# Optimization experiments

Measured on AMD Instinct MI355X. Metric: run time of the kernel, lower is better.

Reference implementation:

```python
import jax, jax.numpy as jnp
import numpy as np
from jax import lax

D_MODEL = 64
D_STATE = 128
D_INNER = 128  # d_model * expand_factor; must equal D_STATE for the original code to broadcast
BATCH = 4
SEQ = 1024
LN_EPS = 1e-5


def setup_inputs() -> dict:
    key = jax.random.key(0)
    ks = jax.random.split(key, 12)
    s = 0.05
    return {
        "x": jax.random.normal(ks[0], (BATCH, SEQ, D_MODEL), jnp.float32),
        "W_in": jax.random.normal(ks[1], (2 * D_INNER, D_MODEL), jnp.float32) * s,
        "W_delta": jax.random.normal(ks[2], (D_INNER, D_MODEL), jnp.float32) * s,
        "b_delta": jax.random.normal(ks[3], (D_INNER,), jnp.float32) * s,
        "W_B": jax.random.normal(ks[4], (D_STATE, D_MODEL), jnp.float32) * s,
        "b_B": jax.random.normal(ks[5], (D_STATE,), jnp.float32) * s,
        "W_C": jax.random.normal(ks[6], (D_STATE, D_MODEL), jnp.float32) * s,
        "b_C": jax.random.normal(ks[7], (D_STATE,), jnp.float32) * s,
        "A": jax.random.normal(ks[8], (D_INNER, D_STATE), jnp.float32) * 0.01,
        "W_out": jax.random.normal(ks[9], (D_MODEL, D_INNER), jnp.float32) * s,
        "ln_w": jnp.ones((D_MODEL,), jnp.float32),
        "ln_b": jnp.zeros((D_MODEL,), jnp.float32),
    }


def _layer_norm(x, w, b):
    mu = x.mean(-1, keepdims=True)
    var = ((x - mu) ** 2).mean(-1, keepdims=True)
    return (x - mu) * lax.rsqrt(var + LN_EPS) * w + b


def reference(x, W_in, W_delta, b_delta, W_B, b_B, W_C, b_C, A, W_out, ln_w, ln_b):
    # projections
    xp = jnp.einsum('bld,ed->ble', x, W_in)            # (B, L, 2*d_inner)
    x_ssm, gate = xp[..., :D_INNER], xp[..., D_INNER:]
    delta = jax.nn.softplus(jnp.einsum('bld,id->bli', x, W_delta) + b_delta)  # (B, L, d_inner)
    Bm = jnp.einsum('bld,sd->bls', x, W_B) + b_B        # (B, L, d_state)
    Cm = jnp.einsum('bld,sd->bls', x, W_C) + b_C        # (B, L, d_state)

    # A_discrete.mean(dim=1): mean over d_inner of exp(delta * A)
    Abar = jnp.exp(delta[..., :, None] * A).mean(axis=2)  # (B, L, d_state)
    x_pool = x_ssm.mean(axis=-1)                          # (B, L) mean over d_inner
    Bx = Bm * x_pool[..., None]                           # (B, L, d_state)

    def step(h, inp):
        a_t, bx_t, c_t = inp                              # each (B, d_state)
        h = a_t * h + bx_t
        y = (c_t * h).sum(axis=-1)                        # (B,)
        return h, y

    h0 = jnp.zeros((x.shape[0], D_STATE), x.dtype)
    _, ys = lax.scan(step, h0,
                     (jnp.swapaxes(Abar, 0, 1), jnp.swapaxes(Bx, 0, 1), jnp.swapaxes(Cm, 0, 1)))
    y = jnp.swapaxes(ys, 0, 1)[..., None]                 # (B, L, 1) -> broadcast over d_inner

    y = y * jax.nn.silu(gate)                             # (B, L, d_inner)
    out = jnp.einsum('bli,di->bld', y, W_out)             # (B, L, d_model)
    return _layer_norm(out + x, ln_w, ln_b)
```

## Files before the change

### kernel.cpp

```cpp
#include <hip/hip_runtime.h>
#include <math.h>

#define NB   4
#define SL   1024
#define NTOK (NB*SL)
#define DM   64
#define DI   128
#define DSt  128
#define SEGLEN 16
#define NSEG (SL/SEGLEN)

#define OFF_GATE   0
#define OFF_DELTA  (OFF_GATE  + NTOK*DI)
#define OFF_BM     (OFF_DELTA + NTOK*DI)
#define OFF_CM     (OFF_BM    + NTOK*DSt)
#define OFF_XPOOL  (OFF_CM    + NTOK*DSt)
#define OFF_ABAR   (OFF_XPOOL + NTOK)
#define OFF_Y      (OFF_ABAR  + NTOK*DSt)
#define OFF_HEND   (OFF_DELTA)
#define OFF_P      (OFF_DELTA + NB*NSEG*DSt)

#define PROJ_TG   128
#define PROJ_TOK  (NTOK/PROJ_TG)

static __device__ __forceinline__ float wave64_sum(float v) {
#pragma unroll
    for (int m = 32; m >= 1; m >>= 1) v += __shfl_xor(v, m, 64);
    return v;
}

__global__ __launch_bounds__(256) void k_proj(
    const float* __restrict__ x, const float* __restrict__ W_in,
    const float* __restrict__ W_delta, const float* __restrict__ b_delta,
    const float* __restrict__ W_B, const float* __restrict__ b_B,
    const float* __restrict__ W_C, const float* __restrict__ b_C,
    float* __restrict__ ws)
{
    __shared__ float xl[PROJ_TOK*DM];
    const int tid = threadIdx.x;
    const int l   = tid & 63;
    const int w   = tid >> 6;
    const int cat = blockIdx.x >> 7;
    const int tg  = blockIdx.x & (PROJ_TG-1);
    const int tok0 = tg * PROJ_TOK;

    {
        const float4* xg = (const float4*)(x + tok0*DM);
        float4* xl4 = (float4*)xl;
        xl4[tid]       = xg[tid];
        xl4[tid + 256] = xg[tid + 256];
    }
    __syncthreads();

    const float* Wbase; const float* bias; float* dst;
    if      (cat == 0) { Wbase = W_in + DI*DM; bias = nullptr; dst = ws + OFF_GATE;  }
    else if (cat == 1) { Wbase = W_delta;      bias = b_delta; dst = ws + OFF_DELTA; }
    else if (cat == 2) { Wbase = W_B;          bias = b_B;     dst = ws + OFF_BM;    }
    else               { Wbase = W_C;          bias = b_C;     dst = ws + OFF_CM;    }

    float4 w0[16], w1[16];
    {
        const float4* Wr0 = (const float4*)(Wbase + l*DM);
        const float4* Wr1 = (const float4*)(Wbase + (l+64)*DM);
#pragma unroll
        for (int k = 0; k < 16; ++k) { w0[k] = Wr0[k]; w1[k] = Wr1[k]; }
    }
    float bias0 = 0.f, bias1 = 0.f;
    if (bias) { bias0 = bias[l]; bias1 = bias[l+64]; }

#pragma unroll 2
    for (int it = 0; it < PROJ_TOK/4; ++it) {
        const int tl = it*4 + w;
        float a0=0.f,a1=0.f,a2=0.f,a3=0.f, c0=0.f,c1=0.f,c2=0.f,c3=0.f;
#pragma unroll
        for (int k = 0; k < 16; ++k) {
            const float4 xv = *(const float4*)(xl + tl*DM + 4*k);
            a0 = fmaf(w0[k].x, xv.x, a0);
            a1 = fmaf(w0[k].y, xv.y, a1);
            a2 = fmaf(w0[k].z, xv.z, a2);
            a3 = fmaf(w0[k].w, xv.w, a3);
            c0 = fmaf(w1[k].x, xv.x, c0);
            c1 = fmaf(w1[k].y, xv.y, c1);
            c2 = fmaf(w1[k].z, xv.z, c2);
            c3 = fmaf(w1[k].w, xv.w, c3);
        }
        float ra = (a0+a1) + (a2+a3) + bias0;
        float rb = (c0+c1) + (c2+c3) + bias1;
        if (cat == 1) {
            ra = fmaxf(ra, 0.f) + log1pf(__expf(-fabsf(ra)));
            rb = fmaxf(rb, 0.f) + log1pf(__expf(-fabsf(rb)));
        }
        const int tok = tok0 + tl;
        dst[tok*128 + l]      = ra;
        dst[tok*128 + 64 + l] = rb;
    }

    if (cat == 0) {
        float wp = 0.f;
#pragma unroll 8
        for (int i = 0; i < DI; ++i) wp += W_in[i*DM + l];
        wp *= (1.0f/DI);
#pragma unroll
        for (int it = 0; it < PROJ_TOK/4; ++it) {
            const int tl = it*4 + w;
            float v = xl[tl*DM + l] * wp;
            v = wave64_sum(v);
            if (l == 0) ws[OFF_XPOOL + tok0 + tl] = v;
        }
    }
}

__global__ __launch_bounds__(256, 2) void k_abar(const float* __restrict__ A,
                                                 float* __restrict__ ws)
{
    const int tid  = threadIdx.x;
    const int s    = tid & 127;
    const int half = tid >> 7;
    float areg[DI];
#pragma unroll
    for (int i = 0; i < DI; ++i) areg[i] = A[i*DSt + s];

    const float* delta = ws + OFF_DELTA;
    float*       Abar  = ws + OFF_ABAR;
    const int base = blockIdx.x * 8 + half * 4;
#pragma unroll
    for (int p = 0; p < 4; ++p) {
        const int tok = base + p;
        const float* dv = delta + tok*DI;
        float a0 = 0.f, a1 = 0.f, a2 = 0.f, a3 = 0.f;
#pragma unroll
        for (int i4 = 0; i4 < DI/4; ++i4) {
            const float4 d4 = *(const float4*)(dv + 4*i4);
            a0 += __expf(d4.x * areg[4*i4    ]);
            a1 += __expf(d4.y * areg[4*i4 + 1]);
            a2 += __expf(d4.z * areg[4*i4 + 2]);
            a3 += __expf(d4.w * areg[4*i4 + 3]);
        }
        Abar[tok*DSt + s] = ((a0+a1) + (a2+a3)) * (1.0f/DI);
    }
}

__global__ __launch_bounds__(128) void k_scan1(float* __restrict__ ws)
{
    const int s   = threadIdx.x;
    const int b   = blockIdx.x >> 6;
    const int seg = blockIdx.x & 63;
    const float* Abar  = ws + OFF_ABAR;
    const float* Bm    = ws + OFF_BM;
    const float* xpool = ws + OFF_XPOOL;
    float h = 0.f, p = 1.f;
    const int t0 = b*SL + seg*SEGLEN;
#pragma unroll
    for (int t = 0; t < SEGLEN; ++t) {
        const float a  = Abar[(t0 + t)*DSt + s];
        const float bx = Bm[(t0 + t)*DSt + s] * xpool[t0 + t];
        h = fmaf(a, h, bx);
        p *= a;
    }
    ws[OFF_HEND + blockIdx.x*DSt + s] = h;
    ws[OFF_P    + blockIdx.x*DSt + s] = p;
}

__global__ __launch_bounds__(128) void k_scan2(float* __restrict__ ws)
{
    __shared__ float prod[SEGLEN][132];
    const int s   = threadIdx.x;
    const int b   = blockIdx.x >> 6;
    const int seg = blockIdx.x & 63;
    const float* Abar  = ws + OFF_ABAR;
    const float* Bm    = ws + OFF_BM;
    const float* Cm    = ws + OFF_CM;
    const float* xpool = ws + OFF_XPOOL;
    const float* hend  = ws + OFF_HEND;
    const float* P     = ws + OFF_P;

    float h = 0.f;
#pragma unroll 4
    for (int j = 0; j < seg; ++j) {
        const int idx = (b*NSEG + j)*DSt + s;
        h = fmaf(P[idx], h, hend[idx]);
    }
    const int t0 = b*SL + seg*SEGLEN;
#pragma unroll
    for (int t = 0; t < SEGLEN; ++t) {
        const float a  = Abar[(t0 + t)*DSt + s];
        const float bx = Bm[(t0 + t)*DSt + s] * xpool[t0 + t];
        h = fmaf(a, h, bx);
        prod[t][s] = Cm[(t0 + t)*DSt + s] * h;
    }
    __syncthreads();
    const int t = s >> 3, r = s & 7;
    float4 acc4 = {0.f,0.f,0.f,0.f};
#pragma unroll
    for (int k4 = 0; k4 < 4; ++k4) {
        const float4 v = *(const float4*)(&prod[t][r*16 + 4*k4]);
        acc4.x += v.x; acc4.y += v.y; acc4.z += v.z; acc4.w += v.w;
    }
    float acc = (acc4.x + acc4.y) + (acc4.z + acc4.w);
#pragma unroll
    for (int m = 1; m <= 4; m <<= 1) acc += __shfl_xor(acc, m, 64);
    if (r == 0) ws[OFF_Y + b*SL + seg*SEGLEN + t] = acc;
}

__global__ __launch_bounds__(256) void k_out(
    const float* __restrict__ x, const float* __restrict__ W_out,
    const float* __restrict__ ln_w, const float* __restrict__ ln_b,
    const float* __restrict__ ws, float* __restrict__ out)
{
    __shared__ float4 Wl[DM*32];
    __shared__ float vbuf[4][DI];
    const int tid = threadIdx.x;
    const int d   = tid & 63;
    const int wv  = tid >> 6;

    const float4* W4g = (const float4*)W_out;
#pragma unroll
    for (int j = 0; j < 8; ++j) {
        const int f = tid + j*256;
        const int row = f >> 5, c4 = f & 31;
        Wl[row*32 + (c4 ^ (row & 7))] = W4g[f];
    }
    __syncthreads();

    const float* gate = ws + OFF_GATE;
    const float* y    = ws + OFF_Y;
    const float lw = ln_w[d], lb = ln_b[d];

#pragma unroll
    for (int it = 0; it < 4; ++it) {
        const int tok = blockIdx.x*16 + it*4 + wv;
        const float yt = y[tok];
        const float g0 = gate[tok*DI + d];
        const float g1 = gate[tok*DI + 64 + d];
        vbuf[wv][d]      = yt * (g0 / (1.f + __expf(-g0)));
        vbuf[wv][64 + d] = yt * (g1 / (1.f + __expf(-g1)));

        float ac0 = 0.f, ac1 = 0.f, ac2 = 0.f, ac3 = 0.f;
#pragma unroll 8
        for (int q = 0; q < 32; ++q) {
            const float4 w  = Wl[d*32 + (q ^ (d & 7))];
            const float4 vv = *(const float4*)(&vbuf[wv][q*4]);
            ac0 = fmaf(w.x, vv.x, ac0);
            ac1 = fmaf(w.y, vv.y, ac1);
            ac2 = fmaf(w.z, vv.z, ac2);
            ac3 = fmaf(w.w, vv.w, ac3);
        }
        const float z  = (ac0+ac1) + (ac2+ac3) + x[tok*DM + d];
        const float s1 = wave64_sum(z);
        const float s2 = wave64_sum(z*z);
        const float mu  = s1 * (1.f/64.f);
        const float var = s2 * (1.f/64.f) - mu*mu;
        out[tok*DM + d] = (z - mu) * rsqrtf(var + 1e-5f) * lw + lb;
    }
}

extern "C" void kernel_launch(void* const* d_in, const int* in_sizes, int n_in,
                              void* d_out, int out_size, void* d_ws, size_t ws_size,
                              hipStream_t stream) {
    const float* x       = (const float*)d_in[0];
    const float* W_in    = (const float*)d_in[1];
    const float* W_delta = (const float*)d_in[2];
    const float* b_delta = (const float*)d_in[3];
    const float* W_B     = (const float*)d_in[4];
    const float* b_B     = (const float*)d_in[5];
    const float* W_C     = (const float*)d_in[6];
    const float* b_C     = (const float*)d_in[7];
    const float* A       = (const float*)d_in[8];
    const float* W_out   = (const float*)d_in[9];
    const float* ln_w    = (const float*)d_in[10];
    const float* ln_b    = (const float*)d_in[11];
    float* out = (float*)d_out;
    float* ws  = (float*)d_ws;

    hipLaunchKernelGGL(k_proj,  dim3(4*PROJ_TG), dim3(256), 0, stream,
                       x, W_in, W_delta, b_delta, W_B, b_B, W_C, b_C, ws);
    hipLaunchKernelGGL(k_abar,  dim3(512),  dim3(256), 0, stream, A, ws);
    hipLaunchKernelGGL(k_scan1, dim3(256),  dim3(128), 0, stream, ws);
    hipLaunchKernelGGL(k_scan2, dim3(256),  dim3(128), 0, stream, ws);
    hipLaunchKernelGGL(k_out,   dim3(256),  dim3(256), 0, stream,
                       x, W_out, ln_w, ln_b, ws, out);
}
```

Baseline: 54.55 us.

## Fuse scan second pass with output projection and stage proj weights in LDS

Merges the scan's second pass with the gated output projection and LayerNorm into one kernel. Per-token y values stay in shared memory instead of a workspace round trip, and one launch is removed. Each block now covers two segments (32 tokens), which halves the grid to 128 blocks and lengthens each block's serial work. The projection kernel also stages its weight tile through swizzled shared memory before loading it into registers, instead of strided per-thread global loads.

Result: faster. 53.26 us (-2.4%).

```diff
diff --git a/kernel.cpp b/kernel.cpp
--- a/kernel.cpp
+++ b/kernel.cpp
@@ -16,12 +16,11 @@
 #define OFF_CM     (OFF_BM    + NTOK*DSt)
 #define OFF_XPOOL  (OFF_CM    + NTOK*DSt)
 #define OFF_ABAR   (OFF_XPOOL + NTOK)
-#define OFF_Y      (OFF_ABAR  + NTOK*DSt)
 #define OFF_HEND   (OFF_DELTA)
 #define OFF_P      (OFF_DELTA + NB*NSEG*DSt)
 
-#define PROJ_TG   128
-#define PROJ_TOK  (NTOK/PROJ_TG)
+#define PROJ_TOK 32
+#define PROJ_TG  (NTOK/PROJ_TOK)
 
 static __device__ __forceinline__ float wave64_sum(float v) {
 #pragma unroll
@@ -36,7 +35,8 @@
     const float* __restrict__ W_C, const float* __restrict__ b_C,
     float* __restrict__ ws)
 {
-    __shared__ float xl[PROJ_TOK*DM];
+    __shared__ float  xl[PROJ_TOK*DM];
+    __shared__ float4 Wl[DI*16];
     const int tid = threadIdx.x;
     const int l   = tid & 63;
     const int w   = tid >> 6;
@@ -44,26 +44,32 @@
     const int tg  = blockIdx.x & (PROJ_TG-1);
     const int tok0 = tg * PROJ_TOK;
 
+    const float* Wbase; const float* bias; float* dst;
+    if      (cat == 0) { Wbase = W_in + DI*DM; bias = nullptr; dst = ws + OFF_GATE;  }
+    else if (cat == 1) { Wbase = W_delta;      bias = b_delta; dst = ws + OFF_DELTA; }
+    else if (cat == 2) { Wbase = W_B;          bias = b_B;     dst = ws + OFF_BM;    }
+    else               { Wbase = W_C;          bias = b_C;     dst = ws + OFF_CM;    }
+
     {
         const float4* xg = (const float4*)(x + tok0*DM);
         float4* xl4 = (float4*)xl;
         xl4[tid]       = xg[tid];
         xl4[tid + 256] = xg[tid + 256];
+        const float4* Wg = (const float4*)Wbase;
+#pragma unroll
+        for (int j = 0; j < 8; ++j) {
+            const int f = tid + j*256;
+            const int row = f >> 4, k = f & 15;
+            Wl[row*16 + (k ^ (row & 15))] = Wg[f];
+        }
     }
     __syncthreads();
 
-    const float* Wbase; const float* bias; float* dst;
-    if      (cat == 0) { Wbase = W_in + DI*DM; bias = nullptr; dst = ws + OFF_GATE;  }
-    else if (cat == 1) { Wbase = W_delta;      bias = b_delta; dst = ws + OFF_DELTA; }
-    else if (cat == 2) { Wbase = W_B;          bias = b_B;     dst = ws + OFF_BM;    }
-    else               { Wbase = W_C;          bias = b_C;     dst = ws + OFF_CM;    }
-
     float4 w0[16], w1[16];
-    {
-        const float4* Wr0 = (const float4*)(Wbase + l*DM);
-        const float4* Wr1 = (const float4*)(Wbase + (l+64)*DM);
-#pragma unroll
-        for (int k = 0; k < 16; ++k) { w0[k] = Wr0[k]; w1[k] = Wr1[k]; }
+#pragma unroll
+    for (int k = 0; k < 16; ++k) {
+        w0[k] = Wl[l*16      + (k ^ (l & 15))];
+        w1[k] = Wl[(l+64)*16 + (k ^ (l & 15))];
     }
     float bias0 = 0.f, bias1 = 0.f;
     if (bias) { bias0 = bias[l]; bias1 = bias[l+64]; }
@@ -161,12 +167,33 @@
     ws[OFF_P    + blockIdx.x*DSt + s] = p;
 }
 
-__global__ __launch_bounds__(128) void k_scan2(float* __restrict__ ws)
-{
-    __shared__ float prod[SEGLEN][132];
-    const int s   = threadIdx.x;
-    const int b   = blockIdx.x >> 6;
-    const int seg = blockIdx.x & 63;
+__global__ __launch_bounds__(256) void k_scan2_out(
+    const float* __restrict__ x, const float* __restrict__ W_out,
+    const float* __restrict__ ln_w, const float* __restrict__ ln_b,
+    float* __restrict__ ws, float* __restrict__ out)
+{
+    __shared__ float  prod[2*SEGLEN][132];
+    __shared__ float4 Wl[DM*32];
+    __shared__ float  vbuf[4][DI];
+    __shared__ float  y_lds[2*SEGLEN];
+
+    const int tid   = threadIdx.x;
+    const int lane  = tid & 63;
+    const int w     = tid >> 6;
+    const int shalf = tid & 127;
+    const int wp    = tid >> 7;
+    const int b     = blockIdx.x >> 5;
+    const int sg    = blockIdx.x & 31;
+    const int seg   = sg*2 + wp;
+
+    const float4* W4g = (const float4*)W_out;
+#pragma unroll
+    for (int j = 0; j < 8; ++j) {
+        const int f = tid + j*256;
+        const int row = f >> 5, c4 = f & 31;
+        Wl[row*32 + (c4 ^ (row & 7))] = W4g[f];
+    }
+
     const float* Abar  = ws + OFF_ABAR;
     const float* Bm    = ws + OFF_BM;
     const float* Cm    = ws + OFF_CM;
@@ -177,73 +204,57 @@
     float h = 0.f;
 #pragma unroll 4
     for (int j = 0; j < seg; ++j) {
-        const int idx = (b*NSEG + j)*DSt + s;
+        const int idx = (b*NSEG + j)*DSt + shalf;
         h = fmaf(P[idx], h, hend[idx]);
     }
     const int t0 = b*SL + seg*SEGLEN;
 #pragma unroll
     for (int t = 0; t < SEGLEN; ++t) {
-        const float a  = Abar[(t0 + t)*DSt + s];
-        const float bx = Bm[(t0 + t)*DSt + s] * xpool[t0 + t];
+        const float a  = Abar[(t0 + t)*DSt + shalf];
+        const float bx = Bm[(t0 + t)*DSt + shalf] * xpool[t0 + t];
         h = fmaf(a, h, bx);
-        prod[t][s] = Cm[(t0 + t)*DSt + s] * h;
+        prod[wp*SEGLEN + t][shalf] = Cm[(t0 + t)*DSt + shalf] * h;
     }
     __syncthreads();
-    const int t = s >> 3, r = s & 7;
-    float4 acc4 = {0.f,0.f,0.f,0.f};
-#pragma unroll
-    for (int k4 = 0; k4 < 4; ++k4) {
-        const float4 v = *(const float4*)(&prod[t][r*16 + 4*k4]);
-        acc4.x += v.x; acc4.y += v.y; acc4.z += v.z; acc4.w += v.w;
-    }
-    float acc = (acc4.x + acc4.y) + (acc4.z + acc4.w);
-#pragma unroll
-    for (int m = 1; m <= 4; m <<= 1) acc += __shfl_xor(acc, m, 64);
-    if (r == 0) ws[OFF_Y + b*SL + seg*SEGLEN + t] = acc;
-}
-
-__global__ __launch_bounds__(256) void k_out(
-    const float* __restrict__ x, const float* __restrict__ W_out,
-    const float* __restrict__ ln_w, const float* __restrict__ ln_b,
-    const float* __restrict__ ws, float* __restrict__ out)
-{
-    __shared__ float4 Wl[DM*32];
-    __shared__ float vbuf[4][DI];
-    const int tid = threadIdx.x;
-    const int d   = tid & 63;
-    const int wv  = tid >> 6;
-
-    const float4* W4g = (const float4*)W_out;
-#pragma unroll
+
+    {
+        const int t = shalf >> 3, r = lane & 7;
+        const int row = wp*SEGLEN + t;
+        float4 acc4 = {0.f,0.f,0.f,0.f};
+#pragma unroll
+        for (int k4 = 0; k4 < 4; ++k4) {
+            const float4 v = *(const float4*)(&prod[row][r*16 + 4*k4]);
+            acc4.x += v.x; acc4.y += v.y; acc4.z += v.z; acc4.w += v.w;
+        }
+        float acc = (acc4.x + acc4.y) + (acc4.z + acc4.w);
+#pragma unroll
+        for (int m = 1; m <= 4; m <<= 1) acc += __shfl_xor(acc, m, 64);
+        if (r == 0) y_lds[row] = acc;
+    }
+    __syncthreads();
+
+    const float* gate = ws + OFF_GATE;
+    const int d = lane;
+    const float lw = ln_w[d], lb = ln_b[d];
+#pragma unroll 2
     for (int j = 0; j < 8; ++j) {
-        const int f = tid + j*256;
-        const int row = f >> 5, c4 = f & 31;
-        Wl[row*32 + (c4 ^ (row & 7))] = W4g[f];
-    }
-    __syncthreads();
-
-    const float* gate = ws + OFF_GATE;
-    const float* y    = ws + OFF_Y;
-    const float lw = ln_w[d], lb = ln_b[d];
-
-#pragma unroll
-    for (int it = 0; it < 4; ++it) {
-        const int tok = blockIdx.x*16 + it*4 + wv;
-        const float yt = y[tok];
+        const int tloc = w*8 + j;
+        const int tok  = b*SL + sg*32 + tloc;
+        const float yt = y_lds[tloc];
         const float g0 = gate[tok*DI + d];
         const float g1 = gate[tok*DI + 64 + d];
-        vbuf[wv][d]      = yt * (g0 / (1.f + __expf(-g0)));
-        vbuf[wv][64 + d] = yt * (g1 / (1.f + __expf(-g1)));
+        vbuf[w][d]      = yt * (g0 / (1.f + __expf(-g0)));
+        vbuf[w][64 + d] = yt * (g1 / (1.f + __expf(-g1)));
 
         float ac0 = 0.f, ac1 = 0.f, ac2 = 0.f, ac3 = 0.f;
 #pragma unroll 8
         for (int q = 0; q < 32; ++q) {
-            const float4 w  = Wl[d*32 + (q ^ (d & 7))];
-            const float4 vv = *(const float4*)(&vbuf[wv][q*4]);
-            ac0 = fmaf(w.x, vv.x, ac0);
-            ac1 = fmaf(w.y, vv.y, ac1);
-            ac2 = fmaf(w.z, vv.z, ac2);
-            ac3 = fmaf(w.w, vv.w, ac3);
+            const float4 wv = Wl[d*32 + (q ^ (d & 7))];
+            const float4 vv = *(const float4*)(&vbuf[w][q*4]);
+            ac0 = fmaf(wv.x, vv.x, ac0);
+            ac1 = fmaf(wv.y, vv.y, ac1);
+            ac2 = fmaf(wv.z, vv.z, ac2);
+            ac3 = fmaf(wv.w, vv.w, ac3);
         }
         const float z  = (ac0+ac1) + (ac2+ac3) + x[tok*DM + d];
         const float s1 = wave64_sum(z);
@@ -272,11 +283,10 @@
     float* out = (float*)d_out;
     float* ws  = (float*)d_ws;
 
-    hipLaunchKernelGGL(k_proj,  dim3(4*PROJ_TG), dim3(256), 0, stream,
+    hipLaunchKernelGGL(k_proj,      dim3(4*PROJ_TG), dim3(256), 0, stream,
                        x, W_in, W_delta, b_delta, W_B, b_B, W_C, b_C, ws);
-    hipLaunchKernelGGL(k_abar,  dim3(512),  dim3(256), 0, stream, A, ws);
-    hipLaunchKernelGGL(k_scan1, dim3(256),  dim3(128), 0, stream, ws);
-    hipLaunchKernelGGL(k_scan2, dim3(256),  dim3(128), 0, stream, ws);
-    hipLaunchKernelGGL(k_out,   dim3(256),  dim3(256), 0, stream,
+    hipLaunchKernelGGL(k_abar,      dim3(512),  dim3(256), 0, stream, A, ws);
+    hipLaunchKernelGGL(k_scan1,     dim3(256),  dim3(128), 0, stream, ws);
+    hipLaunchKernelGGL(k_scan2_out, dim3(128),  dim3(256), 0, stream,
                        x, W_out, ln_w, ln_b, ws, out);
 }
```
